# Kernel tuning notes

Measured on AMD Instinct MI355X. Metric: run time of the kernel, lower is better.

Reference implementation:

```python
import jax, jax.numpy as jnp
import numpy as np

N = 50000   # nodes
E = 800000  # edges
D = 64      # num_filters == hidden_channels
NG = 5      # num_gaussians (edge_attr width, unused by forward math)
NEG_SLOPE = 0.2


def setup_inputs() -> dict:
    key = jax.random.key(0)
    ks = jax.random.split(key, 16)
    s = 1.0 / np.sqrt(D)
    return {
        "x": jax.random.normal(ks[0], (N, D), dtype=jnp.float32),
        "edge_index": jax.random.randint(ks[1], (2, E), 0, N, dtype=jnp.int64),
        "edge_weight": jax.random.uniform(ks[2], (E,), dtype=jnp.float32),
        "edge_attr": jax.random.normal(ks[3], (E, NG), dtype=jnp.float32),
        "W0": jax.random.normal(ks[4], (D, D), dtype=jnp.float32) * s,
        "b0": jnp.zeros((D,), dtype=jnp.float32),
        "W1": jax.random.normal(ks[5], (D, D), dtype=jnp.float32) * s,
        "as1": jax.random.normal(ks[6], (D,), dtype=jnp.float32) * s,
        "ad1": jax.random.normal(ks[7], (D,), dtype=jnp.float32) * s,
        "b1": jnp.zeros((D,), dtype=jnp.float32),
        "W2": jax.random.normal(ks[8], (D, D), dtype=jnp.float32) * s,
        "as2": jax.random.normal(ks[9], (D,), dtype=jnp.float32) * s,
        "ad2": jax.random.normal(ks[10], (D,), dtype=jnp.float32) * s,
        "b2": jnp.zeros((D,), dtype=jnp.float32),
    }


def gat_layer(h, src, dst, W, a_src, a_dst, b):
    # PyG GATConv, heads=1, add_self_loops=False
    hx = h @ W  # [N, D]
    # per-node attention logits, gathered per edge (edge j->i: src=j, dst=i)
    alpha = (hx * a_src).sum(-1)[src] + (hx * a_dst).sum(-1)[dst]  # [E]
    alpha = jax.nn.leaky_relu(alpha, NEG_SLOPE)
    # segment softmax grouped by destination node
    m = jax.ops.segment_max(alpha, dst, num_segments=N)
    e = jnp.exp(alpha - m[dst])
    s = jax.ops.segment_sum(e, dst, num_segments=N)
    p = e / s[dst]  # [E]
    # scatter-add weighted source features
    out = jax.ops.segment_sum(hx[src] * p[:, None], dst, num_segments=N)
    return out + b


def reference(x, edge_index, edge_weight, edge_attr,
              W0, b0, W1, as1, ad1, b1, W2, as2, ad2, b2):
    # edge_weight / edge_attr are accepted but unused, as in the torch module
    src, dst = edge_index[0], edge_index[1]
    out = jax.nn.relu(x @ W0 + b0)
    out = out + jax.nn.relu(gat_layer(out, src, dst, W1, as1, ad1, b1))
    out = out + jax.nn.relu(gat_layer(out, src, dst, W2, as2, ad2, b2))
    return out
```

## Files before the change

### kernel.cpp

```cpp
#include <hip/hip_runtime.h>
#include <hip/hip_bf16.h>

#define DD 64
#define NEG_SLOPE 0.2f
#define HS 68
#define CAP 64
#define BSH 8
#define BN  256
#define NBMAX 256
#define NBLK 256
#define STAGE_CAP 6144

__device__ __forceinline__ unsigned short f2bf(float f)
{
    unsigned u = __float_as_uint(f);
    u += 0x7FFFu + ((u >> 16) & 1u);
    return (unsigned short)(u >> 16);
}
__device__ __forceinline__ float bf2f(unsigned short b)
{
    return __uint_as_float(((unsigned)b) << 16);
}

__global__ __launch_bounds__(256) void mm_fused(
    const float* __restrict__ x,
    const float* __restrict__ W0, const float* __restrict__ b0,
    const float* __restrict__ W1,
    const float* __restrict__ a_src, const float* __restrict__ a_dst,
    float* __restrict__ h, ushort4* __restrict__ hxb4,
    float* __restrict__ sarr, float* __restrict__ darr, int n)
{
    __shared__ float Wsh[DD * DD];
    __shared__ float Hsh[DD * HS];
    int tid = threadIdx.x;
    for (int i = tid * 4; i < DD * DD; i += 1024)
        *(float4*)&Wsh[i] = *(const float4*)&W0[i];

    int fg = tid & 15, ng = tid >> 4;
    int tile0 = blockIdx.x * 64;
    for (int p = 0; p < 4; ++p) {
        int nl = p * 16 + ng, gn = tile0 + nl;
        if (gn < n)
            *(float4*)&Hsh[nl * HS + 4 * fg] = *(const float4*)&x[gn * DD + 4 * fg];
    }
    __syncthreads();

    float4 acc[4];
#pragma unroll
    for (int j = 0; j < 4; ++j) acc[j] = float4{0.f, 0.f, 0.f, 0.f};
#pragma unroll 8
    for (int k = 0; k < DD; ++k) {
        float4 w4 = *(float4*)&Wsh[k * DD + 4 * fg];
#pragma unroll
        for (int j = 0; j < 4; ++j) {
            float hv = Hsh[(4 * ng + j) * HS + k];
            acc[j].x += hv * w4.x; acc[j].y += hv * w4.y;
            acc[j].z += hv * w4.z; acc[j].w += hv * w4.w;
        }
    }

    float4 b4 = *(const float4*)&b0[4 * fg];
    float4 o[4];
#pragma unroll
    for (int j = 0; j < 4; ++j) {
        o[j].x = fmaxf(acc[j].x + b4.x, 0.f);
        o[j].y = fmaxf(acc[j].y + b4.y, 0.f);
        o[j].z = fmaxf(acc[j].z + b4.z, 0.f);
        o[j].w = fmaxf(acc[j].w + b4.w, 0.f);
        int gn = tile0 + 4 * ng + j;
        if (gn < n) *(float4*)&h[gn * DD + 4 * fg] = o[j];
    }
    __syncthreads();

#pragma unroll
    for (int j = 0; j < 4; ++j)
        *(float4*)&Hsh[(4 * ng + j) * HS + 4 * fg] = o[j];
    for (int i = tid * 4; i < DD * DD; i += 1024)
        *(float4*)&Wsh[i] = *(const float4*)&W1[i];
    __syncthreads();

#pragma unroll
    for (int j = 0; j < 4; ++j) acc[j] = float4{0.f, 0.f, 0.f, 0.f};
#pragma unroll 8
    for (int k = 0; k < DD; ++k) {
        float4 w4 = *(float4*)&Wsh[k * DD + 4 * fg];
#pragma unroll
        for (int j = 0; j < 4; ++j) {
            float hv = Hsh[(4 * ng + j) * HS + k];
            acc[j].x += hv * w4.x; acc[j].y += hv * w4.y;
            acc[j].z += hv * w4.z; acc[j].w += hv * w4.w;
        }
    }

    float4 as4 = *(const float4*)&a_src[4 * fg];
    float4 ad4 = *(const float4*)&a_dst[4 * fg];
#pragma unroll
    for (int j = 0; j < 4; ++j) {
        int gn = tile0 + 4 * ng + j;
        if (gn < n) {
            ushort4 hb;
            hb.x = f2bf(acc[j].x); hb.y = f2bf(acc[j].y);
            hb.z = f2bf(acc[j].z); hb.w = f2bf(acc[j].w);
            hxb4[gn * 16 + fg] = hb;
        }
        float ps = acc[j].x * as4.x + acc[j].y * as4.y + acc[j].z * as4.z + acc[j].w * as4.w;
        float pd = acc[j].x * ad4.x + acc[j].y * ad4.y + acc[j].z * ad4.z + acc[j].w * ad4.w;
#pragma unroll
        for (int off = 8; off; off >>= 1) {
            ps += __shfl_xor(ps, off);
            pd += __shfl_xor(pd, off);
        }
        if (fg == 0 && gn < n) { sarr[gn] = ps; darr[gn] = pd; }
    }
}

__global__ __launch_bounds__(256) void mm_gat(
    const float* __restrict__ h, const float* __restrict__ W,
    const float* __restrict__ a_src, const float* __restrict__ a_dst,
    ushort4* __restrict__ hxb4, float* __restrict__ sarr, float* __restrict__ darr,
    int n)
{
    __shared__ float Wsh[DD * DD];
    __shared__ float Hsh[DD * HS];
    int tid = threadIdx.x;
    for (int i = tid * 4; i < DD * DD; i += 1024)
        *(float4*)&Wsh[i] = *(const float4*)&W[i];

    int fg = tid & 15, ng = tid >> 4;
    int tile0 = blockIdx.x * 64;
    for (int p = 0; p < 4; ++p) {
        int nl = p * 16 + ng, gn = tile0 + nl;
        if (gn < n)
            *(float4*)&Hsh[nl * HS + 4 * fg] = *(const float4*)&h[gn * DD + 4 * fg];
    }
    __syncthreads();

    float4 acc[4];
#pragma unroll
    for (int j = 0; j < 4; ++j) acc[j] = float4{0.f, 0.f, 0.f, 0.f};
#pragma unroll 8
    for (int k = 0; k < DD; ++k) {
        float4 w4 = *(float4*)&Wsh[k * DD + 4 * fg];
#pragma unroll
        for (int j = 0; j < 4; ++j) {
            float hv = Hsh[(4 * ng + j) * HS + k];
            acc[j].x += hv * w4.x; acc[j].y += hv * w4.y;
            acc[j].z += hv * w4.z; acc[j].w += hv * w4.w;
        }
    }

    float4 as4 = *(const float4*)&a_src[4 * fg];
    float4 ad4 = *(const float4*)&a_dst[4 * fg];
#pragma unroll
    for (int j = 0; j < 4; ++j) {
        int gn = tile0 + 4 * ng + j;
        if (gn < n) {
            ushort4 hb;
            hb.x = f2bf(acc[j].x); hb.y = f2bf(acc[j].y);
            hb.z = f2bf(acc[j].z); hb.w = f2bf(acc[j].w);
            hxb4[gn * 16 + fg] = hb;
        }
        float ps = acc[j].x * as4.x + acc[j].y * as4.y + acc[j].z * as4.z + acc[j].w * as4.w;
        float pd = acc[j].x * ad4.x + acc[j].y * ad4.y + acc[j].z * ad4.z + acc[j].w * ad4.w;
#pragma unroll
        for (int off = 8; off; off >>= 1) {
            ps += __shfl_xor(ps, off);
            pd += __shfl_xor(pd, off);
        }
        if (fg == 0 && gn < n) { sarr[gn] = ps; darr[gn] = pd; }
    }
}

__device__ __forceinline__ int wave_incl_scan(int v, int lane)
{
#pragma unroll
    for (int off = 1; off < 64; off <<= 1) {
        int t = __shfl_up(v, off);
        if (lane >= off) v += t;
    }
    return v;
}

__global__ __launch_bounds__(512) void chunk_count(
    const int4* __restrict__ dst4, const int* __restrict__ dst,
    int* __restrict__ cnts, int NB, int E4, int E, int C4)
{
    __shared__ int lh[NBMAX];
    int k = blockIdx.x, tid = threadIdx.x;
    for (int i = tid; i < NB; i += 512) lh[i] = 0;
    __syncthreads();
    int i0 = k * C4, i1 = min(i0 + C4, E4);
    for (int i = i0 + tid; i < i1; i += 512) {
        int4 d = dst4[i];
        atomicAdd(&lh[d.x >> BSH], 1);
        atomicAdd(&lh[d.y >> BSH], 1);
        atomicAdd(&lh[d.z >> BSH], 1);
        atomicAdd(&lh[d.w >> BSH], 1);
    }
    if (k == NBLK - 1) {
        for (int e = E4 * 4 + tid; e < E; e += 512)
            atomicAdd(&lh[dst[e] >> BSH], 1);
    }
    __syncthreads();
    for (int i = tid; i < NB; i += 512) cnts[k * NB + i] = lh[i];
}

__global__ __launch_bounds__(256) void csr_scan(
    const int* __restrict__ cnts, int* __restrict__ boff, int* __restrict__ cbase,
    int* __restrict__ row_ptr, int NB, int N, int E)
{
    __shared__ int wsum[4];
    int t = threadIdx.x, lane = t & 63, w = t >> 6;
    int sum = 0;
    if (t < NB)
        for (int k = 0; k < NBLK; ++k) sum += cnts[k * NB + t];
    int incl = wave_incl_scan(sum, lane);
    if (lane == 63) wsum[w] = incl;
    __syncthreads();
    int wo = 0;
    for (int i = 0; i < w; ++i) wo += wsum[i];
    int excl = wo + incl - sum;
    if (t < NB) {
        boff[t] = excl;
        int run = excl;
        for (int k = 0; k < NBLK; ++k) {
            cbase[k * NB + t] = run;
            run += cnts[k * NB + t];
        }
    }
    if (t == 0) { boff[NB] = E; row_ptr[N] = E; }
}

__global__ __launch_bounds__(512) void chunk_scatter(
    const int4* __restrict__ dst4, const int4* __restrict__ src4,
    const int* __restrict__ dst, const int* __restrict__ src,
    const int* __restrict__ cbase, int* __restrict__ ebuf,
    int NB, int E4, int E, int C4)
{
    __shared__ int lcur[NBMAX];
    int k = blockIdx.x, tid = threadIdx.x;
    for (int i = tid; i < NB; i += 512) lcur[i] = cbase[k * NB + i];
    __syncthreads();
    int i0 = k * C4, i1 = min(i0 + C4, E4);
    for (int i = i0 + tid; i < i1; i += 512) {
        int4 d = dst4[i];
        int4 s = src4[i];
        int b, p;
        b = d.x >> BSH; p = atomicAdd(&lcur[b], 1); ebuf[p] = ((d.x & (BN - 1)) << 24) | s.x;
        b = d.y >> BSH; p = atomicAdd(&lcur[b], 1); ebuf[p] = ((d.y & (BN - 1)) << 24) | s.y;
        b = d.z >> BSH; p = atomicAdd(&lcur[b], 1); ebuf[p] = ((d.z & (BN - 1)) << 24) | s.z;
        b = d.w >> BSH; p = atomicAdd(&lcur[b], 1); ebuf[p] = ((d.w & (BN - 1)) << 24) | s.w;
    }
    if (k == NBLK - 1) {
        for (int e = E4 * 4 + tid; e < E; e += 512) {
            int d = dst[e];
            int b = d >> BSH;
            int p = atomicAdd(&lcur[b], 1);
            ebuf[p] = ((d & (BN - 1)) << 24) | src[e];
        }
    }
}

__global__ __launch_bounds__(512) void group_build(
    const int* __restrict__ ebuf, const int* __restrict__ boff,
    int* __restrict__ row_ptr, int* __restrict__ col, int N)
{
    __shared__ int lcnt[BN];
    __shared__ int loff[BN];
    __shared__ int lcur[BN];
    __shared__ int wsum[4];
    __shared__ int stage[STAGE_CAP];
    int b = blockIdx.x, tid = threadIdx.x;
    int e0 = boff[b], e1 = boff[b + 1];
    int total = e1 - e0;
    if (tid < BN) { lcnt[tid] = 0; lcur[tid] = 0; }
    __syncthreads();
    for (int e = e0 + tid; e < e1; e += 512)
        atomicAdd(&lcnt[((unsigned)ebuf[e]) >> 24], 1);
    __syncthreads();
    int lane = tid & 63, w = tid >> 6;
    int v = (tid < BN) ? lcnt[tid] : 0;
    int incl = wave_incl_scan(v, lane);
    if (tid < BN && lane == 63) wsum[w] = incl;
    __syncthreads();
    if (tid < BN) {
        int wo = 0;
        for (int i = 0; i < w; ++i) wo += wsum[i];
        int excl = wo + incl - v;
        loff[tid] = excl;
        int node = b * BN + tid;
        if (node < N) row_ptr[node] = e0 + excl;
    }
    __syncthreads();
    if (total <= STAGE_CAP) {
        for (int e = e0 + tid; e < e1; e += 512) {
            int p = ebuf[e];
            int dl = ((unsigned)p) >> 24;
            int r = atomicAdd(&lcur[dl], 1);
            stage[loff[dl] + r] = p & 0xFFFFFF;
        }
        __syncthreads();
        for (int i = tid; i < total; i += 512)
            col[e0 + i] = stage[i];
    } else {
        for (int e = e0 + tid; e < e1; e += 512) {
            int p = ebuf[e];
            int dl = ((unsigned)p) >> 24;
            int r = atomicAdd(&lcur[dl], 1);
            col[e0 + loff[dl] + r] = p & 0xFFFFFF;
        }
    }
}

__global__ __launch_bounds__(256) void aggregate(
    const ushort4* __restrict__ hxb4, const int* __restrict__ row_ptr,
    const int* __restrict__ col, const float* __restrict__ sarr,
    const float* __restrict__ darr, const float* __restrict__ bias,
    float* __restrict__ h, int n)
{
    __shared__ float aw[4][CAP];
    __shared__ int   ac[4][CAP];
    int tid = threadIdx.x;
    int wid = tid >> 6, lane = tid & 63, fg = lane & 15, es = lane >> 4;
    int v = blockIdx.x * 4 + wid;
    if (v >= n) return;

    int beg = row_ptr[v], end = row_ptr[v + 1];
    int deg = end - beg;
    float adi = darr[v];
    float m = -3.4e38f, s = 0.f;
    float4 acc = float4{0.f, 0.f, 0.f, 0.f};

    if (deg <= CAP) {
        for (int e = beg + lane; e < end; e += 64) {
            int c = col[e];
            float a = sarr[c] + adi;
            a = a > 0.f ? a : NEG_SLOPE * a;
            ac[wid][e - beg] = c;
            aw[wid][e - beg] = a;
            m = fmaxf(m, a);
        }
#pragma unroll
        for (int off = 32; off; off >>= 1) m = fmaxf(m, __shfl_xor(m, off));
        for (int i = lane; i < deg; i += 64) {
            float w = __expf(aw[wid][i] - m);
            aw[wid][i] = w; s += w;
        }
#pragma unroll
        for (int off = 32; off; off >>= 1) s += __shfl_xor(s, off);
#pragma unroll 2
        for (int i = es; i < deg; i += 4) {
            int c = ac[wid][i];
            float w = aw[wid][i];
            ushort4 u = hxb4[c * 16 + fg];
            acc.x += w * bf2f(u.x); acc.y += w * bf2f(u.y);
            acc.z += w * bf2f(u.z); acc.w += w * bf2f(u.w);
        }
    } else {
        for (int e = beg + lane; e < end; e += 64) {
            float a = sarr[col[e]] + adi;
            a = a > 0.f ? a : NEG_SLOPE * a;
            m = fmaxf(m, a);
        }
#pragma unroll
        for (int off = 32; off; off >>= 1) m = fmaxf(m, __shfl_xor(m, off));
        for (int e = beg + lane; e < end; e += 64) {
            float a = sarr[col[e]] + adi;
            a = a > 0.f ? a : NEG_SLOPE * a;
            s += __expf(a - m);
        }
#pragma unroll
        for (int off = 32; off; off >>= 1) s += __shfl_xor(s, off);
        for (int e = beg + es; e < end; e += 4) {
            int c = col[e];
            float a = sarr[c] + adi;
            a = a > 0.f ? a : NEG_SLOPE * a;
            float w = __expf(a - m);
            ushort4 u = hxb4[c * 16 + fg];
            acc.x += w * bf2f(u.x); acc.y += w * bf2f(u.y);
            acc.z += w * bf2f(u.z); acc.w += w * bf2f(u.w);
        }
    }

    acc.x += __shfl_xor(acc.x, 16); acc.y += __shfl_xor(acc.y, 16);
    acc.z += __shfl_xor(acc.z, 16); acc.w += __shfl_xor(acc.w, 16);
    acc.x += __shfl_xor(acc.x, 32); acc.y += __shfl_xor(acc.y, 32);
    acc.z += __shfl_xor(acc.z, 32); acc.w += __shfl_xor(acc.w, 32);

    if (es == 0) {
        float inv = (s > 0.f) ? 1.f / s : 0.f;
        float4 b4 = ((const float4*)bias)[fg];
        float4 o;
        o.x = fmaxf(acc.x * inv + b4.x, 0.f);
        o.y = fmaxf(acc.y * inv + b4.y, 0.f);
        o.z = fmaxf(acc.z * inv + b4.z, 0.f);
        o.w = fmaxf(acc.w * inv + b4.w, 0.f);
        float4* hp = (float4*)&h[v * DD + 4 * fg];
        float4 cur = *hp;
        cur.x += o.x; cur.y += o.y; cur.z += o.z; cur.w += o.w;
        *hp = cur;
    }
}

extern "C" void kernel_launch(void* const* d_in, const int* in_sizes, int n_in,
                              void* d_out, int out_size, void* d_ws, size_t ws_size,
                              hipStream_t stream)
{
    const float* x  = (const float*)d_in[0];
    const int*   ei = (const int*)d_in[1];
    const float* W0 = (const float*)d_in[4];
    const float* b0 = (const float*)d_in[5];
    const float* W1 = (const float*)d_in[6];
    const float* as1= (const float*)d_in[7];
    const float* ad1= (const float*)d_in[8];
    const float* b1 = (const float*)d_in[9];
    const float* W2 = (const float*)d_in[10];
    const float* as2= (const float*)d_in[11];
    const float* ad2= (const float*)d_in[12];
    const float* b2 = (const float*)d_in[13];

    int N = in_sizes[0] / DD;
    int E = in_sizes[1] / 2;
    int E4 = E >> 2;
    int C4 = (E4 + NBLK - 1) / NBLK;
    int NB = (N + BN - 1) >> BSH;
    float* h = (float*)d_out;

    ushort4* hxb4 = (ushort4*)d_ws;
    float* sarr   = (float*)(hxb4 + (size_t)N * 16);
    float* darr   = sarr + N;
    int*   row_ptr= (int*)(darr + N);
    int*   cnts   = row_ptr + (N + 1);
    int*   cbase  = cnts + NBLK * NB;
    int*   boff   = cbase + NBLK * NB;
    int*   ebuf   = boff + (NB + 1);
    int*   colb   = ebuf + E;

    const int* src = ei;
    const int* dst = ei + E;
    const int4* dst4 = (const int4*)dst;
    const int4* src4 = (const int4*)src;

    int mm_tiles = (N + 63) / 64;
    int agg_blks = (N + 3) / 4;

    chunk_count<<<NBLK, 512, 0, stream>>>(dst4, dst, cnts, NB, E4, E, C4);
    csr_scan<<<1, 256, 0, stream>>>(cnts, boff, cbase, row_ptr, NB, N, E);
    chunk_scatter<<<NBLK, 512, 0, stream>>>(dst4, src4, dst, src, cbase, ebuf, NB, E4, E, C4);
    group_build<<<NB, 512, 0, stream>>>(ebuf, boff, row_ptr, colb, N);

    mm_fused<<<mm_tiles, 256, 0, stream>>>(x, W0, b0, W1, as1, ad1, h, hxb4, sarr, darr, N);
    aggregate<<<agg_blks, 256, 0, stream>>>(hxb4, row_ptr, colb, sarr, darr, b1, h, N);

    mm_gat<<<mm_tiles, 256, 0, stream>>>(h, W2, as2, ad2, hxb4, sarr, darr, N);
    aggregate<<<agg_blks, 256, 0, stream>>>(hxb4, row_ptr, colb, sarr, darr, b2, h, N);
}
```

Baseline: 216.7 us.

## Merge edge counting with first matmul; use single-pass online-softmax aggregation

```diff
diff --git a/kernel.cpp b/kernel.cpp
--- a/kernel.cpp
+++ b/kernel.cpp
@@ -4,7 +4,6 @@
 #define DD 64
 #define NEG_SLOPE 0.2f
 #define HS 68
-#define CAP 64
 #define BSH 8
 #define BN  256
 #define NBMAX 256
@@ -17,12 +16,10 @@
     u += 0x7FFFu + ((u >> 16) & 1u);
     return (unsigned short)(u >> 16);
 }
-__device__ __forceinline__ float bf2f(unsigned short b)
-{
-    return __uint_as_float(((unsigned)b) << 16);
-}
-
-__global__ __launch_bounds__(256) void mm_fused(
+
+__global__ __launch_bounds__(256) void k1_count_mm(
+    const int4* __restrict__ dst4, const int* __restrict__ dst,
+    int* __restrict__ cnts, int NB, int E4, int E, int C4,
     const float* __restrict__ x,
     const float* __restrict__ W0, const float* __restrict__ b0,
     const float* __restrict__ W1,
@@ -33,11 +30,34 @@
     __shared__ float Wsh[DD * DD];
     __shared__ float Hsh[DD * HS];
     int tid = threadIdx.x;
+
+    if (blockIdx.x < NBLK) {
+        int* lh = (int*)Wsh;
+        int k = blockIdx.x;
+        for (int i = tid; i < NB; i += 256) lh[i] = 0;
+        __syncthreads();
+        int i0 = k * C4, i1 = min(i0 + C4, E4);
+        for (int i = i0 + tid; i < i1; i += 256) {
+            int4 d = dst4[i];
+            atomicAdd(&lh[d.x >> BSH], 1);
+            atomicAdd(&lh[d.y >> BSH], 1);
+            atomicAdd(&lh[d.z >> BSH], 1);
+            atomicAdd(&lh[d.w >> BSH], 1);
+        }
+        if (k == NBLK - 1) {
+            for (int e = E4 * 4 + tid; e < E; e += 256)
+                atomicAdd(&lh[dst[e] >> BSH], 1);
+        }
+        __syncthreads();
+        for (int i = tid; i < NB; i += 256) cnts[k * NB + i] = lh[i];
+        return;
+    }
+
     for (int i = tid * 4; i < DD * DD; i += 1024)
         *(float4*)&Wsh[i] = *(const float4*)&W0[i];
 
     int fg = tid & 15, ng = tid >> 4;
-    int tile0 = blockIdx.x * 64;
+    int tile0 = (blockIdx.x - NBLK) * 64;
     for (int p = 0; p < 4; ++p) {
         int nl = p * 16 + ng, gn = tile0 + nl;
         if (gn < n)
@@ -179,30 +199,6 @@
         if (lane >= off) v += t;
     }
     return v;
-}
-
-__global__ __launch_bounds__(512) void chunk_count(
-    const int4* __restrict__ dst4, const int* __restrict__ dst,
-    int* __restrict__ cnts, int NB, int E4, int E, int C4)
-{
-    __shared__ int lh[NBMAX];
-    int k = blockIdx.x, tid = threadIdx.x;
-    for (int i = tid; i < NB; i += 512) lh[i] = 0;
-    __syncthreads();
-    int i0 = k * C4, i1 = min(i0 + C4, E4);
-    for (int i = i0 + tid; i < i1; i += 512) {
-        int4 d = dst4[i];
-        atomicAdd(&lh[d.x >> BSH], 1);
-        atomicAdd(&lh[d.y >> BSH], 1);
-        atomicAdd(&lh[d.z >> BSH], 1);
-        atomicAdd(&lh[d.w >> BSH], 1);
-    }
-    if (k == NBLK - 1) {
-        for (int e = E4 * 4 + tid; e < E; e += 512)
-            atomicAdd(&lh[dst[e] >> BSH], 1);
-    }
-    __syncthreads();
-    for (int i = tid; i < NB; i += 512) cnts[k * NB + i] = lh[i];
 }
 
 __global__ __launch_bounds__(256) void csr_scan(
@@ -313,92 +309,86 @@
 }
 
 __global__ __launch_bounds__(256) void aggregate(
-    const ushort4* __restrict__ hxb4, const int* __restrict__ row_ptr,
+    const uint4* __restrict__ hxq, const int* __restrict__ row_ptr,
     const int* __restrict__ col, const float* __restrict__ sarr,
     const float* __restrict__ darr, const float* __restrict__ bias,
     float* __restrict__ h, int n)
 {
-    __shared__ float aw[4][CAP];
-    __shared__ int   ac[4][CAP];
     int tid = threadIdx.x;
-    int wid = tid >> 6, lane = tid & 63, fg = lane & 15, es = lane >> 4;
+    int wid = tid >> 6, lane = tid & 63;
+    int fl = lane & 7, es = lane >> 3;
     int v = blockIdx.x * 4 + wid;
     if (v >= n) return;
 
     int beg = row_ptr[v], end = row_ptr[v + 1];
-    int deg = end - beg;
     float adi = darr[v];
     float m = -3.4e38f, s = 0.f;
-    float4 acc = float4{0.f, 0.f, 0.f, 0.f};
-
-    if (deg <= CAP) {
-        for (int e = beg + lane; e < end; e += 64) {
-            int c = col[e];
-            float a = sarr[c] + adi;
-            a = a > 0.f ? a : NEG_SLOPE * a;
-            ac[wid][e - beg] = c;
-            aw[wid][e - beg] = a;
-            m = fmaxf(m, a);
-        }
-#pragma unroll
-        for (int off = 32; off; off >>= 1) m = fmaxf(m, __shfl_xor(m, off));
-        for (int i = lane; i < deg; i += 64) {
-            float w = __expf(aw[wid][i] - m);
-            aw[wid][i] = w; s += w;
-        }
-#pragma unroll
-        for (int off = 32; off; off >>= 1) s += __shfl_xor(s, off);
-#pragma unroll 2
-        for (int i = es; i < deg; i += 4) {
-            int c = ac[wid][i];
-            float w = aw[wid][i];
-            ushort4 u = hxb4[c * 16 + fg];
-            acc.x += w * bf2f(u.x); acc.y += w * bf2f(u.y);
-            acc.z += w * bf2f(u.z); acc.w += w * bf2f(u.w);
-        }
-    } else {
-        for (int e = beg + lane; e < end; e += 64) {
-            float a = sarr[col[e]] + adi;
-            a = a > 0.f ? a : NEG_SLOPE * a;
-            m = fmaxf(m, a);
-        }
-#pragma unroll
-        for (int off = 32; off; off >>= 1) m = fmaxf(m, __shfl_xor(m, off));
-        for (int e = beg + lane; e < end; e += 64) {
-            float a = sarr[col[e]] + adi;
-            a = a > 0.f ? a : NEG_SLOPE * a;
-            s += __expf(a - m);
-        }
-#pragma unroll
-        for (int off = 32; off; off >>= 1) s += __shfl_xor(s, off);
-        for (int e = beg + es; e < end; e += 4) {
-            int c = col[e];
-            float a = sarr[c] + adi;
-            a = a > 0.f ? a : NEG_SLOPE * a;
-            float w = __expf(a - m);
-            ushort4 u = hxb4[c * 16 + fg];
-            acc.x += w * bf2f(u.x); acc.y += w * bf2f(u.y);
-            acc.z += w * bf2f(u.z); acc.w += w * bf2f(u.w);
-        }
-    }
-
-    acc.x += __shfl_xor(acc.x, 16); acc.y += __shfl_xor(acc.y, 16);
-    acc.z += __shfl_xor(acc.z, 16); acc.w += __shfl_xor(acc.w, 16);
-    acc.x += __shfl_xor(acc.x, 32); acc.y += __shfl_xor(acc.y, 32);
-    acc.z += __shfl_xor(acc.z, 32); acc.w += __shfl_xor(acc.w, 32);
+    float acc[8];
+#pragma unroll
+    for (int j = 0; j < 8; ++j) acc[j] = 0.f;
+
+    for (int e = beg + es; e < end; e += 8) {
+        int c = col[e];
+        float a = sarr[c] + adi;
+        a = a > 0.f ? a : NEG_SLOPE * a;
+        uint4 u = hxq[c * 8 + fl];
+        float mN = fmaxf(m, a);
+        float f = __expf(m - mN);
+        float wgt = __expf(a - mN);
+        m = mN;
+        s = s * f + wgt;
+        float p0 = __uint_as_float(u.x << 16);
+        float p1 = __uint_as_float(u.x & 0xffff0000u);
+        float p2 = __uint_as_float(u.y << 16);
+        float p3 = __uint_as_float(u.y & 0xffff0000u);
+        float p4 = __uint_as_float(u.z << 16);
+        float p5 = __uint_as_float(u.z & 0xffff0000u);
+        float p6 = __uint_as_float(u.w << 16);
+        float p7 = __uint_as_float(u.w & 0xffff0000u);
+        acc[0] = acc[0] * f + wgt * p0;
+        acc[1] = acc[1] * f + wgt * p1;
+        acc[2] = acc[2] * f + wgt * p2;
+        acc[3] = acc[3] * f + wgt * p3;
+        acc[4] = acc[4] * f + wgt * p4;
+        acc[5] = acc[5] * f + wgt * p5;
+        acc[6] = acc[6] * f + wgt * p6;
+        acc[7] = acc[7] * f + wgt * p7;
+    }
+
+#pragma unroll
+    for (int off = 8; off < 64; off <<= 1) {
+        float m2 = __shfl_xor(m, off);
+        float s2 = __shfl_xor(s, off);
+        float mN = fmaxf(m, m2);
+        float f1 = __expf(m - mN);
+        float f2 = __expf(m2 - mN);
+        s = s * f1 + s2 * f2;
+#pragma unroll
+        for (int j = 0; j < 8; ++j) {
+            float a2 = __shfl_xor(acc[j], off);
+            acc[j] = acc[j] * f1 + a2 * f2;
+        }
+        m = mN;
+    }
 
     if (es == 0) {
         float inv = (s > 0.f) ? 1.f / s : 0.f;
-        float4 b4 = ((const float4*)bias)[fg];
-        float4 o;
-        o.x = fmaxf(acc.x * inv + b4.x, 0.f);
-        o.y = fmaxf(acc.y * inv + b4.y, 0.f);
-        o.z = fmaxf(acc.z * inv + b4.z, 0.f);
-        o.w = fmaxf(acc.w * inv + b4.w, 0.f);
-        float4* hp = (float4*)&h[v * DD + 4 * fg];
-        float4 cur = *hp;
-        cur.x += o.x; cur.y += o.y; cur.z += o.z; cur.w += o.w;
-        *hp = cur;
+        float* hp = &h[v * DD + fl * 8];
+        float4 c0 = *(float4*)hp;
+        float4 c1 = *(float4*)(hp + 4);
+        const float* bp = &bias[fl * 8];
+        float4 b0 = *(const float4*)bp;
+        float4 b1 = *(const float4*)(bp + 4);
+        c0.x += fmaxf(acc[0] * inv + b0.x, 0.f);
+        c0.y += fmaxf(acc[1] * inv + b0.y, 0.f);
+        c0.z += fmaxf(acc[2] * inv + b0.z, 0.f);
+        c0.w += fmaxf(acc[3] * inv + b0.w, 0.f);
+        c1.x += fmaxf(acc[4] * inv + b1.x, 0.f);
+        c1.y += fmaxf(acc[5] * inv + b1.y, 0.f);
+        c1.z += fmaxf(acc[6] * inv + b1.z, 0.f);
+        c1.w += fmaxf(acc[7] * inv + b1.w, 0.f);
+        *(float4*)hp = c0;
+        *(float4*)(hp + 4) = c1;
     }
 }
 
@@ -444,14 +434,16 @@
     int mm_tiles = (N + 63) / 64;
     int agg_blks = (N + 3) / 4;
 
-    chunk_count<<<NBLK, 512, 0, stream>>>(dst4, dst, cnts, NB, E4, E, C4);
+    k1_count_mm<<<NBLK + mm_tiles, 256, 0, stream>>>(
+        dst4, dst, cnts, NB, E4, E, C4,
+        x, W0, b0, W1, as1, ad1, h, hxb4, sarr, darr, N);
+
     csr_scan<<<1, 256, 0, stream>>>(cnts, boff, cbase, row_ptr, NB, N, E);
     chunk_scatter<<<NBLK, 512, 0, stream>>>(dst4, src4, dst, src, cbase, ebuf, NB, E4, E, C4);
     group_build<<<NB, 512, 0, stream>>>(ebuf, boff, row_ptr, colb, N);
 
-    mm_fused<<<mm_tiles, 256, 0, stream>>>(x, W0, b0, W1, as1, ad1, h, hxb4, sarr, darr, N);
-    aggregate<<<agg_blks, 256, 0, stream>>>(hxb4, row_ptr, colb, sarr, darr, b1, h, N);
+    aggregate<<<agg_blks, 256, 0, stream>>>((const uint4*)hxb4, row_ptr, colb, sarr, darr, b1, h, N);
 
     mm_gat<<<mm_tiles, 256, 0, stream>>>(h, W2, as2, ad2, hxb4, sarr, darr, N);
-    aggregate<<<agg_blks, 256, 0, stream>>>(hxb4, row_ptr, colb, sarr, darr, b2, h, N);
-}
+    aggregate<<<agg_blks, 256, 0, stream>>>((const uint4*)hxb4, row_ptr, colb, sarr, darr, b2, h, N);
+}
```

New measurement: 219.4 us. About the same (+1.2%).
